# Kernel tuning notes

Measured on AMD Instinct MI355X. Metric: run time of the kernel, lower is better.

Reference implementation:

```python
import jax, jax.numpy as jnp
import numpy as np

WS = 8       # window_size
SHIFT = 4    # shift_size
NH = 6       # num_heads
C = 192      # dim
EPS = 1e-5


def _rel_index(ws):
    # standard Swin relative position index, [ws*ws, ws*ws]
    coords = np.stack(np.meshgrid(np.arange(ws), np.arange(ws), indexing='ij')).reshape(2, -1)
    rel = coords[:, :, None] - coords[:, None, :]            # [2, N, N]
    rel = rel.transpose(1, 2, 0) + (ws - 1)                  # shift to >= 0
    return rel[..., 0] * (2 * ws - 1) + rel[..., 1]          # [N, N]


def _attn_mask(h, w, ws, shift):
    # shifted-window attention mask, [nW, N, N] with 0 / -100
    img = np.zeros((h, w), dtype=np.float32)
    cnt = 0
    for hs in (slice(0, -ws), slice(-ws, -shift), slice(-shift, None)):
        for wsl in (slice(0, -ws), slice(-ws, -shift), slice(-shift, None)):
            img[hs, wsl] = cnt
            cnt += 1
    mw = img.reshape(h // ws, ws, w // ws, ws).transpose(0, 2, 1, 3).reshape(-1, ws * ws)
    diff = mw[:, None, :] - mw[:, :, None]
    return np.where(diff != 0, -100.0, 0.0).astype(np.float32)


def _ln(x, g, b):
    m = x.mean(-1, keepdims=True)
    v = ((x - m) ** 2).mean(-1, keepdims=True)
    return (x - m) / jnp.sqrt(v + EPS) * g + b


def setup_inputs() -> dict:
    key = jax.random.key(0)
    ks = jax.random.split(key, 16)
    B, H, W = 32, 64, 64
    Ch = 4 * C
    s = 0.02
    return {
        'x': jax.random.normal(ks[0], (B, H * W, C), jnp.float32),
        'h': H,
        'w': W,
        'norm1_g': jnp.ones((C,), jnp.float32),
        'norm1_b': jnp.zeros((C,), jnp.float32),
        'qkv_w': jax.random.normal(ks[1], (3 * C, C), jnp.float32) * s,
        'qkv_b': jnp.zeros((3 * C,), jnp.float32),
        'rpb_table': jax.random.normal(ks[2], ((2 * WS - 1) ** 2, NH), jnp.float32) * s,
        'proj_w': jax.random.normal(ks[3], (C, C), jnp.float32) * s,
        'proj_b': jnp.zeros((C,), jnp.float32),
        'norm2_g': jnp.ones((C,), jnp.float32),
        'norm2_b': jnp.zeros((C,), jnp.float32),
        'fc1_w': jax.random.normal(ks[4], (Ch, C), jnp.float32) * s,
        'fc1_b': jnp.zeros((Ch,), jnp.float32),
        'fc2_w': jax.random.normal(ks[5], (C, Ch), jnp.float32) * s,
        'fc2_b': jnp.zeros((C,), jnp.float32),
    }


def reference(x, h, w, norm1_g, norm1_b, qkv_w, qkv_b, rpb_table, proj_w, proj_b,
              norm2_g, norm2_b, fc1_w, fc1_b, fc2_w, fc2_b):
    B, L, _ = x.shape
    N = WS * WS
    hd = C // NH
    scale = hd ** -0.5
    nW = (h // WS) * (w // WS)

    shortcut = x
    xn = _ln(x, norm1_g, norm1_b).reshape(B, h, w, C)
    xs = jnp.roll(xn, (-SHIFT, -SHIFT), (1, 2))
    # window partition -> [B*nW, N, C]
    xw = xs.reshape(B, h // WS, WS, w // WS, WS, C).transpose(0, 1, 3, 2, 4, 5).reshape(-1, N, C)

    qkv = (xw @ qkv_w.T + qkv_b).reshape(-1, N, 3, NH, hd).transpose(2, 0, 3, 1, 4)
    q, k, v = qkv[0], qkv[1], qkv[2]                          # [B*nW, NH, N, hd]
    attn = jnp.einsum('whnd,whmd->whnm', q * scale, k)        # [B*nW, NH, N, N]
    bias = rpb_table[jnp.asarray(_rel_index(WS))].transpose(2, 0, 1)  # [NH, N, N]
    attn = attn + bias[None]
    mask = jnp.asarray(_attn_mask(h, w, WS, SHIFT))           # [nW, N, N]
    attn = attn.reshape(B, nW, NH, N, N) + mask[None, :, None]
    attn = jax.nn.softmax(attn.reshape(-1, NH, N, N), axis=-1)
    out = jnp.einsum('whnm,whmd->whnd', attn, v).transpose(0, 2, 1, 3).reshape(-1, N, C)
    out = out @ proj_w.T + proj_b

    # window reverse + unroll
    out = out.reshape(B, h // WS, w // WS, WS, WS, C).transpose(0, 1, 3, 2, 4, 5).reshape(B, h, w, C)
    out = jnp.roll(out, (SHIFT, SHIFT), (1, 2)).reshape(B, h * w, C)

    x = shortcut + out
    xn = _ln(x, norm2_g, norm2_b)
    mlp = jax.nn.gelu(xn @ fc1_w.T + fc1_b, approximate=False) @ fc2_w.T + fc2_b
    return x + mlp
```

## Files before the change

### kernel.cpp

```cpp
#include <hip/hip_runtime.h>
#include <hip/hip_bf16.h>
#include <math.h>

typedef __bf16 bf16;
typedef __bf16 bf16x8 __attribute__((ext_vector_type(8)));
typedef float f32x4 __attribute__((ext_vector_type(4)));

#define BATCH 32
#define HW 64
#define L 4096
#define CDIM 192
#define NHEADS 6
#define HD 32
#define NTOK 131072
#define QKVC 576
#define CH 768

template <bool PERM, typename TIN>
__global__ __launch_bounds__(256) void ln_kernel(const TIN* __restrict__ xin,
                                                 const float* __restrict__ g,
                                                 const float* __restrict__ bta,
                                                 bf16* __restrict__ yout) {
  int wave = threadIdx.x >> 6;
  int lane = threadIdx.x & 63;
  int tok = blockIdx.x * 4 + wave;
  int src;
  if (PERM) {
    int win = tok >> 6;
    int n = tok & 63;
    int bb = win >> 6;
    int wid = win & 63;
    int i = ((wid >> 3) << 3) + (n >> 3);
    int j = ((wid & 7) << 3) + (n & 7);
    int sh = (i + 4) & 63;
    int sw = (j + 4) & 63;
    src = bb * L + sh * HW + sw;
  } else {
    src = tok;
  }
  const TIN* sp = xin + (size_t)src * CDIM;
  float v0 = (float)sp[lane];
  float v1 = (float)sp[lane + 64];
  float v2 = (float)sp[lane + 128];
  float s = v0 + v1 + v2;
#pragma unroll
  for (int off = 32; off; off >>= 1) s += __shfl_xor(s, off, 64);
  float mean = s * (1.0f / 192.0f);
  float d0 = v0 - mean, d1 = v1 - mean, d2 = v2 - mean;
  float q = d0 * d0 + d1 * d1 + d2 * d2;
#pragma unroll
  for (int off = 32; off; off >>= 1) q += __shfl_xor(q, off, 64);
  float rstd = rsqrtf(q * (1.0f / 192.0f) + 1e-5f);
  bf16* dp = yout + (size_t)tok * CDIM;
  dp[lane]       = (bf16)(d0 * rstd * g[lane]       + bta[lane]);
  dp[lane + 64]  = (bf16)(d1 * rstd * g[lane + 64]  + bta[lane + 64]);
  dp[lane + 128] = (bf16)(d2 * rstd * g[lane + 128] + bta[lane + 128]);
}

template <int EPI, typename TR, typename TO>
__global__ __launch_bounds__(256) void gemm_bt(const bf16* __restrict__ A,
                                               const float* __restrict__ W,
                                               const float* __restrict__ bias,
                                               const TR* __restrict__ res,
                                               TO* __restrict__ Cout,
                                               int M, int N, int K, int ldw) {
  __shared__ alignas(16) bf16 As[128 * 32];
  __shared__ alignas(16) bf16 Bs[64 * 32];
  const int n0 = blockIdx.x * 64;
  const int m0 = blockIdx.y * 128;
  const int tid = threadIdx.x;
  const int lane = tid & 63;
  const int wave = tid >> 6;
  const int wm = (wave >> 1) * 64;
  const int wn = (wave & 1) * 32;
  const int lr = lane & 15;
  const int quad = lane >> 4;

  f32x4 acc[4][2];
#pragma unroll
  for (int i = 0; i < 4; i++)
#pragma unroll
    for (int j = 0; j < 2; j++) acc[i][j] = (f32x4){0.f, 0.f, 0.f, 0.f};

  const int arow = tid >> 2;
  const int akq = (tid & 3) * 8;

  for (int k0 = 0; k0 < K; k0 += 32) {
    const bf16* Ap = A + (size_t)(m0 + arow) * K + k0 + akq;
    *(uint4*)(&As[arow * 32 + akq]) = *(const uint4*)Ap;
    *(uint4*)(&As[(arow + 64) * 32 + akq]) = *(const uint4*)(Ap + (size_t)64 * K);
    const float* Wp = W + (size_t)(n0 + arow) * ldw + k0 + akq;
    float4 w0 = *(const float4*)Wp;
    float4 w1 = *(const float4*)(Wp + 4);
    bf16x8 bw;
    bw[0] = (bf16)w0.x; bw[1] = (bf16)w0.y; bw[2] = (bf16)w0.z; bw[3] = (bf16)w0.w;
    bw[4] = (bf16)w1.x; bw[5] = (bf16)w1.y; bw[6] = (bf16)w1.z; bw[7] = (bf16)w1.w;
    *(bf16x8*)(&Bs[arow * 32 + akq]) = bw;
    __syncthreads();

    bf16x8 af[4], bfr[2];
#pragma unroll
    for (int mi = 0; mi < 4; mi++)
      af[mi] = *(const bf16x8*)(&As[(wm + mi * 16 + lr) * 32 + quad * 8]);
#pragma unroll
    for (int nj = 0; nj < 2; nj++)
      bfr[nj] = *(const bf16x8*)(&Bs[(wn + nj * 16 + lr) * 32 + quad * 8]);
#pragma unroll
    for (int mi = 0; mi < 4; mi++)
#pragma unroll
      for (int nj = 0; nj < 2; nj++)
        acc[mi][nj] = __builtin_amdgcn_mfma_f32_16x16x32_bf16(af[mi], bfr[nj],
                                                              acc[mi][nj], 0, 0, 0);
    __syncthreads();
  }

#pragma unroll
  for (int mi = 0; mi < 4; mi++) {
#pragma unroll
    for (int nj = 0; nj < 2; nj++) {
      int col = n0 + wn + nj * 16 + lr;
      float bv = bias[col];
#pragma unroll
      for (int r = 0; r < 4; r++) {
        int row = m0 + wm + mi * 16 + quad * 4 + r;
        float v = acc[mi][nj][r] + bv;
        size_t didx;
        if (EPI == 3) {
          int win = row >> 6, n = row & 63;
          int bb = win >> 6, wid = win & 63;
          int i = ((wid >> 3) << 3) + (n >> 3);
          int j = ((wid & 7) << 3) + (n & 7);
          int fi = (i + 4) & 63;
          int fj = (j + 4) & 63;
          didx = ((size_t)(bb * L + fi * HW + fj)) * (size_t)N + col;
          v += (float)res[didx];
        } else {
          didx = (size_t)row * N + col;
        }
        Cout[didx] = (TO)v;
      }
    }
  }
}

__device__ __forceinline__ int region64(int h) {
  return (h < 56) ? 0 : ((h < 60) ? 1 : 2);
}

__global__ __launch_bounds__(64) void attn_kernel(const bf16* __restrict__ qkv,
                                                  const float* __restrict__ rpb,
                                                  bf16* __restrict__ out) {
  __shared__ alignas(16) bf16 Qs[64 * 32];
  __shared__ alignas(16) bf16 Ks[64 * 32];
  __shared__ alignas(16) bf16 Vt[32 * 64];
  __shared__ alignas(16) bf16 Ps[64 * 64];
  const int win = blockIdx.x;
  const int head = blockIdx.y;
  const int lane = threadIdx.x;
  const int lr = lane & 15;
  const int quad = lane >> 4;
  const int wid = win & 63;
  const int wi = wid >> 3, wj = wid & 7;

  const bf16* base = qkv + (size_t)win * 64 * QKVC + head * HD;
#pragma unroll
  for (int rep = 0; rep < 4; rep++) {
    int r = (lane >> 2) + rep * 16;
    int c = (lane & 3) * 8;
    *(uint4*)(&Qs[r * 32 + c]) = *(const uint4*)(base + (size_t)r * QKVC + c);
    *(uint4*)(&Ks[r * 32 + c]) = *(const uint4*)(base + CDIM + (size_t)r * QKVC + c);
    uint4 vv = *(const uint4*)(base + 2 * CDIM + (size_t)r * QKVC + c);
    bf16x8 v8 = __builtin_bit_cast(bf16x8, vv);
#pragma unroll
    for (int j = 0; j < 8; j++) Vt[(c + j) * 64 + r] = v8[j];
  }
  __syncthreads();

  f32x4 s[4][4];
  {
    bf16x8 qf[4], kf[4];
#pragma unroll
    for (int mi = 0; mi < 4; mi++)
      qf[mi] = *(const bf16x8*)(&Qs[(mi * 16 + lr) * 32 + quad * 8]);
#pragma unroll
    for (int nj = 0; nj < 4; nj++)
      kf[nj] = *(const bf16x8*)(&Ks[(nj * 16 + lr) * 32 + quad * 8]);
#pragma unroll
    for (int mi = 0; mi < 4; mi++)
#pragma unroll
      for (int nj = 0; nj < 4; nj++)
        s[mi][nj] = __builtin_amdgcn_mfma_f32_16x16x32_bf16(
            qf[mi], kf[nj], (f32x4){0.f, 0.f, 0.f, 0.f}, 0, 0, 0);
  }

  const float scale = 0.17677669529663687f;
#pragma unroll
  for (int mi = 0; mi < 4; mi++) {
#pragma unroll
    for (int nj = 0; nj < 4; nj++) {
#pragma unroll
      for (int r = 0; r < 4; r++) {
        int rr = mi * 16 + quad * 4 + r;
        int cc = nj * 16 + lr;
        int qi = rr >> 3, qj = rr & 7, ki = cc >> 3, kj = cc & 7;
        int idx = (qi - ki + 7) * 15 + (qj - kj + 7);
        float bv = rpb[idx * NHEADS + head];
        int regr = 3 * region64(wi * 8 + qi) + region64(wj * 8 + qj);
        int regc = 3 * region64(wi * 8 + ki) + region64(wj * 8 + kj);
        float mv = (regr != regc) ? -100.0f : 0.0f;
        s[mi][nj][r] = s[mi][nj][r] * scale + bv + mv;
      }
    }
  }

#pragma unroll
  for (int mi = 0; mi < 4; mi++) {
#pragma unroll
    for (int r = 0; r < 4; r++) {
      float mx = s[mi][0][r];
#pragma unroll
      for (int nj = 1; nj < 4; nj++) mx = fmaxf(mx, s[mi][nj][r]);
#pragma unroll
      for (int off = 1; off < 16; off <<= 1) mx = fmaxf(mx, __shfl_xor(mx, off, 64));
      float sum = 0.f;
#pragma unroll
      for (int nj = 0; nj < 4; nj++) {
        float p = __expf(s[mi][nj][r] - mx);
        s[mi][nj][r] = p;
        sum += p;
      }
#pragma unroll
      for (int off = 1; off < 16; off <<= 1) sum += __shfl_xor(sum, off, 64);
      float inv = 1.0f / sum;
#pragma unroll
      for (int nj = 0; nj < 4; nj++) s[mi][nj][r] *= inv;
    }
  }

#pragma unroll
  for (int mi = 0; mi < 4; mi++)
#pragma unroll
    for (int nj = 0; nj < 4; nj++)
#pragma unroll
      for (int r = 0; r < 4; r++)
        Ps[(mi * 16 + quad * 4 + r) * 64 + nj * 16 + lr] = (bf16)s[mi][nj][r];
  __syncthreads();

  f32x4 o[4][2];
#pragma unroll
  for (int mi = 0; mi < 4; mi++)
#pragma unroll
    for (int nj = 0; nj < 2; nj++) o[mi][nj] = (f32x4){0.f, 0.f, 0.f, 0.f};
#pragma unroll
  for (int ks = 0; ks < 2; ks++) {
    bf16x8 pf[4], vf[2];
#pragma unroll
    for (int mi = 0; mi < 4; mi++)
      pf[mi] = *(const bf16x8*)(&Ps[(mi * 16 + lr) * 64 + ks * 32 + quad * 8]);
#pragma unroll
    for (int nj = 0; nj < 2; nj++)
      vf[nj] = *(const bf16x8*)(&Vt[(nj * 16 + lr) * 64 + ks * 32 + quad * 8]);
#pragma unroll
    for (int mi = 0; mi < 4; mi++)
#pragma unroll
      for (int nj = 0; nj < 2; nj++)
        o[mi][nj] = __builtin_amdgcn_mfma_f32_16x16x32_bf16(pf[mi], vf[nj],
                                                            o[mi][nj], 0, 0, 0);
  }

#pragma unroll
  for (int mi = 0; mi < 4; mi++)
#pragma unroll
    for (int nj = 0; nj < 2; nj++)
#pragma unroll
      for (int r = 0; r < 4; r++) {
        size_t row = (size_t)win * 64 + mi * 16 + quad * 4 + r;
        int col = head * HD + nj * 16 + lr;
        out[row * CDIM + col] = (bf16)o[mi][nj][r];
      }
}

__global__ __launch_bounds__(256) void wconv_kernel(const float* __restrict__ fc1w,
                                                    const float* __restrict__ fc2w,
                                                    bf16* __restrict__ W1b,
                                                    bf16* __restrict__ W2b) {
  int i = blockIdx.x * 256 + threadIdx.x;
  W1b[i] = (bf16)fc1w[i];
  int c = i / 12288;
  int rem = i - c * 12288;
  int n = rem >> 6;
  int k = rem & 63;
  W2b[i] = (bf16)fc2w[n * 768 + c * 64 + k];
}

__global__ __launch_bounds__(512, 4) void mlp_fused(
    const bf16* __restrict__ Xn,
    const bf16* __restrict__ W1b,
    const bf16* __restrict__ W2b,
    const float* __restrict__ b1,
    const float* __restrict__ b2,
    const bf16* __restrict__ X1,
    float* __restrict__ out) {
  __shared__ alignas(16) bf16 W1s[64 * 192];
  __shared__ alignas(16) bf16 W2s[192 * 64];
  __shared__ alignas(16) bf16 Hs[8][16 * 64];

  const int tid = threadIdx.x;
  const int lane = tid & 63;
  const int wave = tid >> 6;
  const int lr = lane & 15;
  const int quad = lane >> 4;
  const int m0 = blockIdx.x * 128;
  const int arow = m0 + wave * 16 + lr;

  bf16x8 aF[6];
  {
    const bf16* ap = Xn + (size_t)arow * CDIM + quad * 8;
#pragma unroll
    for (int ks = 0; ks < 6; ks++)
      aF[ks] = *(const bf16x8*)(ap + ks * 32);
  }

  f32x4 oacc[12];
#pragma unroll
  for (int nt = 0; nt < 12; nt++) oacc[nt] = (f32x4){0.f, 0.f, 0.f, 0.f};

  for (int c = 0; c < 12; c++) {
    const int h0 = c * 64;
#pragma unroll
    for (int i = 0; i < 3; i++) {
      int u = i * 512 + tid;
      int row = u / 24;
      int c8 = u - row * 24;
      int c8s = (c8 & ~7) | ((c8 & 7) ^ (row & 7));
      *(uint4*)(&W1s[row * 192 + c8s * 8]) =
          *(const uint4*)(W1b + (size_t)(h0 + row) * 192 + c8 * 8);
    }
#pragma unroll
    for (int i = 0; i < 3; i++) {
      int u = i * 512 + tid;
      int row = u >> 3;
      int g = u & 7;
      int gs = g ^ (row & 7);
      *(uint4*)(&W2s[row * 64 + gs * 8]) =
          *(const uint4*)(W2b + (size_t)c * 12288 + row * 64 + g * 8);
    }
    __syncthreads();

    f32x4 hacc[4];
#pragma unroll
    for (int nj = 0; nj < 4; nj++) hacc[nj] = (f32x4){0.f, 0.f, 0.f, 0.f};
#pragma unroll
    for (int ks = 0; ks < 6; ks++) {
      int c8 = ks * 4 + quad;
      int base = (c8 & ~7) | ((c8 & 7) ^ (lr & 7));
#pragma unroll
      for (int nj = 0; nj < 4; nj++) {
        bf16x8 bF = *(const bf16x8*)(&W1s[(nj * 16 + lr) * 192 + base * 8]);
        hacc[nj] = __builtin_amdgcn_mfma_f32_16x16x32_bf16(aF[ks], bF, hacc[nj], 0, 0, 0);
      }
    }

#pragma unroll
    for (int nj = 0; nj < 4; nj++) {
      float bh = b1[h0 + nj * 16 + lr];
#pragma unroll
      for (int r = 0; r < 4; r++) {
        float h = hacc[nj][r] + bh;
        float gl = 0.5f * h * (1.0f + erff(h * 0.70710678118654752f));
        int hr = quad * 4 + r;
        int col = nj * 16 + lr;
        int c8 = col >> 3;
        int c8s = c8 ^ (hr & 7);
        Hs[wave][hr * 64 + c8s * 8 + (col & 7)] = (bf16)gl;
      }
    }

#pragma unroll
    for (int ks = 0; ks < 2; ks++) {
      int c8 = ks * 4 + quad;
      int c8s = c8 ^ (lr & 7);
      bf16x8 hF = *(const bf16x8*)(&Hs[wave][lr * 64 + c8s * 8]);
#pragma unroll
      for (int nt = 0; nt < 12; nt++) {
        bf16x8 wF = *(const bf16x8*)(&W2s[(nt * 16 + lr) * 64 + c8s * 8]);
        oacc[nt] = __builtin_amdgcn_mfma_f32_16x16x32_bf16(hF, wF, oacc[nt], 0, 0, 0);
      }
    }
    __syncthreads();
  }

#pragma unroll
  for (int nt = 0; nt < 12; nt++) {
    float fb = b2[nt * 16 + lr];
#pragma unroll
    for (int r = 0; r < 4; r++) {
      size_t row = (size_t)(m0 + wave * 16 + quad * 4 + r);
      size_t idx = row * CDIM + nt * 16 + lr;
      out[idx] = oacc[nt][r] + fb + (float)X1[idx];
    }
  }
}

extern "C" void kernel_launch(void* const* d_in, const int* in_sizes, int n_in,
                              void* d_out, int out_size, void* d_ws, size_t ws_size,
                              hipStream_t stream) {
  const float* x      = (const float*)d_in[0];
  const float* n1g    = (const float*)d_in[3];
  const float* n1b    = (const float*)d_in[4];
  const float* qkv_w  = (const float*)d_in[5];
  const float* qkv_b  = (const float*)d_in[6];
  const float* rpb    = (const float*)d_in[7];
  const float* proj_w = (const float*)d_in[8];
  const float* proj_b = (const float*)d_in[9];
  const float* n2g    = (const float*)d_in[10];
  const float* n2b    = (const float*)d_in[11];
  const float* fc1_w  = (const float*)d_in[12];
  const float* fc1_b  = (const float*)d_in[13];
  const float* fc2_w  = (const float*)d_in[14];
  const float* fc2_b  = (const float*)d_in[15];
  float* out = (float*)d_out;

  char* wsb = (char*)d_ws;
  bf16* Q   = (bf16*)wsb;
  bf16* X1  = (bf16*)wsb;
  bf16* W1b = (bf16*)(wsb + 52428800ull);
  bf16* W2b = (bf16*)(wsb + 52428800ull + 294912ull);
  bf16* T   = (bf16*)(wsb + 150994944ull);

  ln_kernel<true, float><<<32768, 256, 0, stream>>>(x, n1g, n1b, T);
  gemm_bt<0, float, bf16><<<dim3(9, 1024), 256, 0, stream>>>(
      T, qkv_w, qkv_b, nullptr, Q, NTOK, QKVC, CDIM, CDIM);
  attn_kernel<<<dim3(2048, 6), 64, 0, stream>>>(Q, rpb, T);
  gemm_bt<3, float, bf16><<<dim3(3, 1024), 256, 0, stream>>>(
      T, proj_w, proj_b, x, X1, NTOK, CDIM, CDIM, CDIM);
  wconv_kernel<<<576, 256, 0, stream>>>(fc1_w, fc2_w, W1b, W2b);
  ln_kernel<false, bf16><<<32768, 256, 0, stream>>>(X1, n2g, n2b, T);
  mlp_fused<<<1024, 512, 0, stream>>>(T, W1b, W2b, fc1_b, fc2_b, X1, out);
}
```

Before: 589.1 us.

## Pre-swizzle MLP weights and stream them via direct global-to-LDS loads; cheaper erf

The weight conversion kernel now writes fc1/fc2 bf16 weights already XOR-swizzled in the order the LDS layout expects. That lets the fused MLP kernel copy each 24 KB weight chunk with global_load_lds, a direct global-to-LDS transfer that bypasses registers and the per-thread index arithmetic. The exact erff inside GELU is also replaced by the Abramowitz-Stegun polynomial with __expf, which lowers ALU cost. That approximation has an absolute error around 1e-7, within bf16 tolerance but no longer exact.

New measurement: 584.1 us. About the same (-0.9%).

```diff
diff --git a/kernel.cpp b/kernel.cpp
--- a/kernel.cpp
+++ b/kernel.cpp
@@ -5,6 +5,9 @@
 typedef __bf16 bf16;
 typedef __bf16 bf16x8 __attribute__((ext_vector_type(8)));
 typedef float f32x4 __attribute__((ext_vector_type(4)));
+
+typedef const __attribute__((address_space(1))) char gchar;
+typedef __attribute__((address_space(3))) char lchar;
 
 #define BATCH 32
 #define HW 64
@@ -285,12 +288,22 @@
                                                     bf16* __restrict__ W1b,
                                                     bf16* __restrict__ W2b) {
   int i = blockIdx.x * 256 + threadIdx.x;
-  W1b[i] = (bf16)fc1w[i];
-  int c = i / 12288;
-  int rem = i - c * 12288;
-  int n = rem >> 6;
-  int k = rem & 63;
-  W2b[i] = (bf16)fc2w[n * 768 + c * 64 + k];
+  {
+    int h = i / 192;
+    int cc = i - h * 192;
+    int gs = cc >> 3, e = cc & 7;
+    int g = (gs & ~7) | ((gs & 7) ^ (h & 7));
+    W1b[i] = (bf16)fc1w[h * 192 + g * 8 + e];
+  }
+  {
+    int c = i / 12288;
+    int rem = i - c * 12288;
+    int n = rem >> 6;
+    int cc = rem & 63;
+    int gs = cc >> 3, e = cc & 7;
+    int g = gs ^ (n & 7);
+    W2b[i] = (bf16)fc2w[n * 768 + c * 64 + g * 8 + e];
+  }
 }
 
 __global__ __launch_bounds__(512, 4) void mlp_fused(
@@ -327,23 +340,20 @@
 
   for (int c = 0; c < 12; c++) {
     const int h0 = c * 64;
-#pragma unroll
-    for (int i = 0; i < 3; i++) {
-      int u = i * 512 + tid;
-      int row = u / 24;
-      int c8 = u - row * 24;
-      int c8s = (c8 & ~7) | ((c8 & 7) ^ (row & 7));
-      *(uint4*)(&W1s[row * 192 + c8s * 8]) =
-          *(const uint4*)(W1b + (size_t)(h0 + row) * 192 + c8 * 8);
-    }
-#pragma unroll
-    for (int i = 0; i < 3; i++) {
-      int u = i * 512 + tid;
-      int row = u >> 3;
-      int g = u & 7;
-      int gs = g ^ (row & 7);
-      *(uint4*)(&W2s[row * 64 + gs * 8]) =
-          *(const uint4*)(W2b + (size_t)c * 12288 + row * 64 + g * 8);
+    {
+      const size_t cb = (size_t)c * 24576;
+      const int off = wave * 1024 + lane * 16;
+      const char* g1 = (const char*)W1b + cb + off;
+      const char* g2 = (const char*)W2b + cb + off;
+      char* l1 = (char*)W1s + wave * 1024;
+      char* l2 = (char*)W2s + wave * 1024;
+#pragma unroll
+      for (int i = 0; i < 3; i++) {
+        __builtin_amdgcn_global_load_lds((gchar*)(g1 + i * 8192),
+                                         (lchar*)(l1 + i * 8192), 16, 0, 0);
+        __builtin_amdgcn_global_load_lds((gchar*)(g2 + i * 8192),
+                                         (lchar*)(l2 + i * 8192), 16, 0, 0);
+      }
     }
     __syncthreads();
 
@@ -367,7 +377,15 @@
 #pragma unroll
       for (int r = 0; r < 4; r++) {
         float h = hacc[nj][r] + bh;
-        float gl = 0.5f * h * (1.0f + erff(h * 0.70710678118654752f));
+        float x = fabsf(h) * 0.70710678118654752f;
+        float t = __fdividef(1.0f, fmaf(0.3275911f, x, 1.0f));
+        float p = t * (0.254829592f +
+                  t * (-0.284496736f +
+                  t * (1.421413741f +
+                  t * (-1.453152027f + t * 1.061405429f))));
+        float er = fmaf(-p, __expf(-x * x), 1.0f);
+        er = copysignf(er, h);
+        float gl = 0.5f * h * (1.0f + er);
         int hr = quad * 4 + r;
         int col = nj * 16 + lr;
         int c8 = col >> 3;
```
